# Optimization experiments

Measured on AMD Instinct MI355X. Metric: run time of the kernel, lower is better.

Reference implementation:

```python
import jax, jax.numpy as jnp
import numpy as np

B, T, H, UNITS = 64, 512, 1024, 1024

def setup_inputs() -> dict:
    key = jax.random.key(0)
    ks = jax.random.split(key, 8)
    s = 0.02
    return {
        "dec_hidden": jax.random.normal(ks[0], (B, H), jnp.float32),
        "enc_output": jax.random.normal(ks[1], (B, T, H), jnp.float32),
        "Wh": jax.random.normal(ks[2], (H, UNITS), jnp.float32) * s,
        "bh": jnp.zeros((UNITS,), jnp.float32),
        "Ws": jax.random.normal(ks[3], (H, UNITS), jnp.float32) * s,
        "bs": jnp.zeros((UNITS,), jnp.float32),
        "Wv": jax.random.normal(ks[4], (UNITS, 1), jnp.float32) * s,
        "bv": jnp.zeros((1,), jnp.float32),
    }

def reference(dec_hidden, enc_output, Wh, bh, Ws, bs, Wv, bv):
    # Faithful to original: tanh applied only to W_h(enc_output) term.
    enc_proj = jnp.tanh(jnp.einsum('bth,hu->btu', enc_output, Wh) + bh)  # [B,T,U]
    dec_proj = (dec_hidden @ Ws + bs)[:, None, :]                        # [B,1,U]
    score = jnp.einsum('btu,uo->bto', enc_proj + dec_proj, Wv) + bv      # [B,T,1]
    attn_dist = jax.nn.softmax(score, axis=1)                            # [B,T,1]
    context_vector = jnp.sum(attn_dist * enc_output, axis=1)             # [B,H]
    return context_vector, jnp.squeeze(attn_dist, axis=-1)
```

## Files before the change

### kernel.cpp

```cpp
#include <hip/hip_runtime.h>
#include <hip/hip_bf16.h>

typedef unsigned short u16;
typedef __attribute__((ext_vector_type(8))) short short8;
typedef __attribute__((ext_vector_type(4))) float f32x4;

#define B_  64
#define T_  512
#define H_  1024
#define U_  1024
#define BT_ (B_*T_)

#define BM 256
#define BN 256
#define BK 32

#define GLL16(gp, lp) __builtin_amdgcn_global_load_lds( \
    (const __attribute__((address_space(1))) void*)(gp), \
    (__attribute__((address_space(3))) void*)(lp), 16, 0, 0)

template<int N>
__device__ __forceinline__ void vwait() {
  asm volatile("s_waitcnt vmcnt(%0)" :: "n"(N) : "memory");
}

__device__ __forceinline__ u16 f32_to_bf16(float f) {
  union { float f; unsigned u; } v; v.f = f;
  unsigned r = v.u + 0x7FFFu + ((v.u >> 16) & 1u);
  return (u16)(r >> 16);
}
__device__ __forceinline__ unsigned pack_bf16x2(float lo, float hi) {
  return (unsigned)f32_to_bf16(lo) | ((unsigned)f32_to_bf16(hi) << 16);
}

__global__ __launch_bounds__(256) void ba_prep(const float4* __restrict__ in,
                                               uint4* __restrict__ out,
                                               const float* __restrict__ wh,
                                               u16* __restrict__ whT,
                                               float* __restrict__ score) {
  __shared__ float tile[32][33];
  const int bx = blockIdx.x;
  const int tid = threadIdx.x;
  if (bx < 16384) {
    int i = bx * 256 + tid;
    float4 v0 = in[2 * i], v1 = in[2 * i + 1];
    uint4 o;
    o.x = pack_bf16x2(v0.x, v0.y);
    o.y = pack_bf16x2(v0.z, v0.w);
    o.z = pack_bf16x2(v1.x, v1.y);
    o.w = pack_bf16x2(v1.z, v1.w);
    out[i] = o;
    if (bx < 128) score[bx * 256 + tid] = 0.f;
  } else {
    int wb = bx - 16384;
    int u0 = (wb & 31) * 32, h0 = (wb >> 5) * 32;
    int tx = tid & 31, ty = tid >> 5;
    #pragma unroll
    for (int i = 0; i < 32; i += 8)
      tile[ty + i][tx] = wh[(long)(h0 + ty + i) * U_ + u0 + tx];
    __syncthreads();
    #pragma unroll
    for (int i = 0; i < 32; i += 8)
      whT[(long)(u0 + ty + i) * H_ + h0 + tx] = f32_to_bf16(tile[tx][ty + i]);
  }
}

__global__ __launch_bounds__(512, 2) void ba_score(
    const u16* __restrict__ A, const u16* __restrict__ Bt,
    const float* __restrict__ bh, const float* __restrict__ wv,
    float* __restrict__ score) {
  __shared__ u16 lA[4][BM * BK];
  __shared__ u16 lB[4][BN * BK];

  const int tid  = threadIdx.x;
  const int wid  = tid >> 6;
  const int lane = tid & 63;
  const int wm = wid >> 2;
  const int wn = wid & 3;
  const long row0  = (long)blockIdx.x * BM;
  const int  ncol0 = blockIdx.y * BN;

  const int srow = tid >> 2;
  const int csw  = (((tid & 3) - ((tid >> 3) & 3)) & 3) * 8;

  const int fr = lane & 15;
  const int pofs = (((lane >> 4) + ((lane >> 1) & 3)) & 3) * 8;
  const int aBase = (wm * 128 + fr) * BK + pofs;
  const int bBase = (wn * 64  + fr) * BK + pofs;

  const u16* gA = A  + (row0 + srow) * H_ + csw;
  const u16* gB = Bt + (long)(ncol0 + srow) * H_ + csw;

  f32x4 acc[8][4];
  #pragma unroll
  for (int i = 0; i < 8; ++i)
    #pragma unroll
    for (int j = 0; j < 4; ++j) acc[i][j] = (f32x4){0.f, 0.f, 0.f, 0.f};

#define STAGEF(t_, b_) do { \
    const long _k = (long)(t_) * BK; \
    GLL16(gA + _k,            (char*)lA[b_] + wid * 1024); \
    GLL16(gA + 128 * H_ + _k, (char*)lA[b_] + 8192 + wid * 1024); \
    GLL16(gB + _k,            (char*)lB[b_] + wid * 1024); \
    GLL16(gB + 128 * H_ + _k, (char*)lB[b_] + 8192 + wid * 1024); \
  } while (0)

#define TILE(t_, WAITN, DO_STAGE) do { \
    const int _bt = (t_) & 3; \
    vwait<WAITN>(); \
    __builtin_amdgcn_sched_barrier(0); \
    __builtin_amdgcn_s_barrier(); \
    __builtin_amdgcn_sched_barrier(0); \
    short8 bfrag[4], afrag[4]; \
    _Pragma("unroll") \
    for (int nf = 0; nf < 4; ++nf) \
      bfrag[nf] = *(const short8*)&lB[_bt][bBase + nf * 512]; \
    _Pragma("unroll") \
    for (int mf = 0; mf < 4; ++mf) \
      afrag[mf] = *(const short8*)&lA[_bt][aBase + mf * 512]; \
    if (DO_STAGE) { \
      const long _k = (long)((t_) + 3) * BK; \
      const int _nb = ((t_) + 3) & 3; \
      GLL16(gA + _k,            (char*)lA[_nb] + wid * 1024); \
      GLL16(gA + 128 * H_ + _k, (char*)lA[_nb] + 8192 + wid * 1024); \
    } \
    __builtin_amdgcn_s_setprio(1); \
    _Pragma("unroll") \
    for (int mf = 0; mf < 4; ++mf) \
      _Pragma("unroll") \
      for (int nf = 0; nf < 4; ++nf) \
        acc[mf][nf] = __builtin_amdgcn_mfma_f32_16x16x32_bf16(afrag[mf], bfrag[nf], acc[mf][nf], 0, 0, 0); \
    __builtin_amdgcn_s_setprio(0); \
    _Pragma("unroll") \
    for (int mf = 0; mf < 4; ++mf) \
      afrag[mf] = *(const short8*)&lA[_bt][aBase + (4 + mf) * 512]; \
    if (DO_STAGE) { \
      const long _k = (long)((t_) + 3) * BK; \
      const int _nb = ((t_) + 3) & 3; \
      GLL16(gB + _k,            (char*)lB[_nb] + wid * 1024); \
      GLL16(gB + 128 * H_ + _k, (char*)lB[_nb] + 8192 + wid * 1024); \
    } \
    __builtin_amdgcn_s_setprio(1); \
    _Pragma("unroll") \
    for (int mf = 0; mf < 4; ++mf) \
      _Pragma("unroll") \
      for (int nf = 0; nf < 4; ++nf) \
        acc[4 + mf][nf] = __builtin_amdgcn_mfma_f32_16x16x32_bf16(afrag[mf], bfrag[nf], acc[4 + mf][nf], 0, 0, 0); \
    __builtin_amdgcn_s_setprio(0); \
  } while (0)

  STAGEF(0, 0);
  STAGEF(1, 1);
  STAGEF(2, 2);

  for (int t = 0; t < 30; ++t) {
    TILE(t, 8, t < 29);
  }
  TILE(30, 4, false);
  TILE(31, 0, false);
#undef TILE
#undef STAGEF

  float sloc[8][4];
  #pragma unroll
  for (int mf = 0; mf < 8; ++mf)
    #pragma unroll
    for (int r = 0; r < 4; ++r) sloc[mf][r] = 0.f;

  #pragma unroll
  for (int nf = 0; nf < 4; ++nf) {
    const int n = ncol0 + wn * 64 + nf * 16 + fr;
    const float bhn = bh[n];
    const float wvn = wv[n];
    #pragma unroll
    for (int mf = 0; mf < 8; ++mf) {
      #pragma unroll
      for (int r = 0; r < 4; ++r) {
        float x = acc[mf][nf][r] + bhn;
        float e = __expf(2.f * x);
        sloc[mf][r] += (1.f - 2.f / (e + 1.f)) * wvn;
      }
    }
  }

  #pragma unroll
  for (int mf = 0; mf < 8; ++mf) {
    #pragma unroll
    for (int r = 0; r < 4; ++r) {
      float v = sloc[mf][r];
      v += __shfl_xor(v, 1);
      v += __shfl_xor(v, 2);
      v += __shfl_xor(v, 4);
      v += __shfl_xor(v, 8);
      if ((lane & 15) == 0) {
        long m = row0 + wm * 128 + mf * 16 + (lane >> 4) * 4 + r;
        atomicAdd(&score[m], v);
      }
    }
  }
}

__global__ __launch_bounds__(256) void ba_context1(const float4* __restrict__ enc4,
                                                   const float* __restrict__ score,
                                                   float* __restrict__ attn_out,
                                                   float4* __restrict__ part) {
  __shared__ float redm[4], reds[4];
  __shared__ float atile[32];
  int b = blockIdx.x, c = blockIdx.y, tid = threadIdx.x;
  int lane = tid & 63, wid = tid >> 6;
  const float* s = score + b * T_;
  float v0 = s[tid], v1 = s[tid + 256];
  float m = fmaxf(v0, v1);
  #pragma unroll
  for (int o = 1; o < 64; o <<= 1) m = fmaxf(m, __shfl_xor(m, o));
  if (lane == 0) redm[wid] = m;
  __syncthreads();
  m = fmaxf(fmaxf(redm[0], redm[1]), fmaxf(redm[2], redm[3]));
  float e0 = __expf(v0 - m), e1 = __expf(v1 - m);
  float sum = e0 + e1;
  #pragma unroll
  for (int o = 1; o < 64; o <<= 1) sum += __shfl_xor(sum, o);
  if (lane == 0) reds[wid] = sum;
  __syncthreads();
  float inv = 1.f / (reds[0] + reds[1] + reds[2] + reds[3]);

  if (c == 0) {
    attn_out[b * T_ + tid] = e0 * inv;
    attn_out[b * T_ + tid + 256] = e1 * inv;
  }
  int base = c * 32;
  if (base < 256) {
    if (tid >= base && tid < base + 32) atile[tid - base] = e0 * inv;
  } else {
    int bb = base - 256;
    if (tid >= bb && tid < bb + 32) atile[tid - bb] = e1 * inv;
  }
  __syncthreads();

  const float4* e = enc4 + ((long)b * T_ + base) * (H_ / 4) + tid;
  float4 acc = {0.f, 0.f, 0.f, 0.f};
  #pragma unroll 4
  for (int t = 0; t < 32; ++t) {
    float4 v = e[(long)t * (H_ / 4)];
    float at = atile[t];
    acc.x = fmaf(at, v.x, acc.x);
    acc.y = fmaf(at, v.y, acc.y);
    acc.z = fmaf(at, v.z, acc.z);
    acc.w = fmaf(at, v.w, acc.w);
  }
  part[((long)b * 16 + c) * (H_ / 4) + tid] = acc;
}

__global__ __launch_bounds__(256) void ba_context2(const float4* __restrict__ part,
                                                   float4* __restrict__ ctx) {
  int b = blockIdx.x;
  int tid = threadIdx.x;
  const float4* p = part + (long)b * 16 * (H_ / 4) + tid;
  float4 acc = {0.f, 0.f, 0.f, 0.f};
  #pragma unroll
  for (int c = 0; c < 16; ++c) {
    float4 v = p[c * (H_ / 4)];
    acc.x += v.x; acc.y += v.y; acc.z += v.z; acc.w += v.w;
  }
  ctx[b * (H_ / 4) + tid] = acc;
}

extern "C" void kernel_launch(void* const* d_in, const int* in_sizes, int n_in,
                              void* d_out, int out_size, void* d_ws, size_t ws_size,
                              hipStream_t stream) {
  const float* enc = (const float*)d_in[1];
  const float* Wh  = (const float*)d_in[2];
  const float* bh  = (const float*)d_in[3];
  const float* Wv  = (const float*)d_in[6];

  float* out      = (float*)d_out;
  float* ctx_out  = out;
  float* attn_out = out + B_ * H_;

  char* ws = (char*)d_ws;
  u16*   encb  = (u16*)ws;
  u16*   whT   = (u16*)(ws + (size_t)67108864);
  float* score = (float*)(ws + (size_t)67108864 + 2097152);
  float* part  = (float*)(ws + (size_t)67108864 + 2097152 + 131072);

  ba_prep<<<16384 + 1024, 256, 0, stream>>>((const float4*)enc, (uint4*)encb,
                                            Wh, whT, score);
  ba_score<<<dim3(BT_ / BM, U_ / BN), 512, 0, stream>>>(encb, whT, bh, Wv, score);
  ba_context1<<<dim3(B_, 16), 256, 0, stream>>>((const float4*)enc, score,
                                                attn_out, (float4*)part);
  ba_context2<<<B_, 256, 0, stream>>>((const float4*)part, (float4*)ctx_out);
}
```

Before: 323.0 us.

## Switch score GEMM from 16x16x32 to 32x32x16 bf16 MFMA tiles

Replaces the 16x16x32 bf16 MFMA instruction with 32x32x16, reorganising each wave's 128x64 tile into 4x2 fragments of 32x32 with 16-wide accumulators. LDS fragment addressing, the k-half split within BK=32, and the epilogue row mapping and shuffle reduction (now across 32 lanes) are all reworked to match the new output layout. The larger MFMA shape halves the number of fragment loads per tile and may issue more efficiently, at the cost of a new LDS access pattern whose bank behaviour and swizzle correctness are less certain.

```diff
diff --git a/kernel.cpp b/kernel.cpp
--- a/kernel.cpp
+++ b/kernel.cpp
@@ -3,7 +3,7 @@
 
 typedef unsigned short u16;
 typedef __attribute__((ext_vector_type(8))) short short8;
-typedef __attribute__((ext_vector_type(4))) float f32x4;
+typedef __attribute__((ext_vector_type(16))) float f32x16;
 
 #define B_  64
 #define T_  512
@@ -83,19 +83,21 @@
   const int srow = tid >> 2;
   const int csw  = (((tid & 3) - ((tid >> 3) & 3)) & 3) * 8;
 
-  const int fr = lane & 15;
-  const int pofs = (((lane >> 4) + ((lane >> 1) & 3)) & 3) * 8;
-  const int aBase = (wm * 128 + fr) * BK + pofs;
-  const int bBase = (wn * 64  + fr) * BK + pofs;
+  const int l31 = lane & 31;
+  const int rowA = (wm * 128 + l31) * BK;
+  const int rowB = (wn * 64  + l31) * BK;
+  const int s0 = (((lane >> 5) + ((lane >> 1) & 3)) & 3) * 8;
 
   const u16* gA = A  + (row0 + srow) * H_ + csw;
   const u16* gB = Bt + (long)(ncol0 + srow) * H_ + csw;
 
-  f32x4 acc[8][4];
-  #pragma unroll
-  for (int i = 0; i < 8; ++i)
-    #pragma unroll
-    for (int j = 0; j < 4; ++j) acc[i][j] = (f32x4){0.f, 0.f, 0.f, 0.f};
+  f32x16 acc[4][2];
+  #pragma unroll
+  for (int i = 0; i < 4; ++i)
+    #pragma unroll
+    for (int j = 0; j < 2; ++j)
+      #pragma unroll
+      for (int r = 0; r < 16; ++r) acc[i][j][r] = 0.f;
 
 #define STAGEF(t_, b_) do { \
     const long _k = (long)(t_) * BK; \
@@ -111,13 +113,13 @@
     __builtin_amdgcn_sched_barrier(0); \
     __builtin_amdgcn_s_barrier(); \
     __builtin_amdgcn_sched_barrier(0); \
-    short8 bfrag[4], afrag[4]; \
-    _Pragma("unroll") \
-    for (int nf = 0; nf < 4; ++nf) \
-      bfrag[nf] = *(const short8*)&lB[_bt][bBase + nf * 512]; \
-    _Pragma("unroll") \
-    for (int mf = 0; mf < 4; ++mf) \
-      afrag[mf] = *(const short8*)&lA[_bt][aBase + mf * 512]; \
+    short8 af[4], bfr[2]; \
+    _Pragma("unroll") \
+    for (int mf = 0; mf < 4; ++mf) \
+      af[mf] = *(const short8*)&lA[_bt][rowA + mf * 1024 + s0]; \
+    _Pragma("unroll") \
+    for (int nf = 0; nf < 2; ++nf) \
+      bfr[nf] = *(const short8*)&lB[_bt][rowB + nf * 1024 + s0]; \
     if (DO_STAGE) { \
       const long _k = (long)((t_) + 3) * BK; \
       const int _nb = ((t_) + 3) & 3; \
@@ -128,12 +130,15 @@
     _Pragma("unroll") \
     for (int mf = 0; mf < 4; ++mf) \
       _Pragma("unroll") \
-      for (int nf = 0; nf < 4; ++nf) \
-        acc[mf][nf] = __builtin_amdgcn_mfma_f32_16x16x32_bf16(afrag[mf], bfrag[nf], acc[mf][nf], 0, 0, 0); \
+      for (int nf = 0; nf < 2; ++nf) \
+        acc[mf][nf] = __builtin_amdgcn_mfma_f32_32x32x16_bf16(af[mf], bfr[nf], acc[mf][nf], 0, 0, 0); \
     __builtin_amdgcn_s_setprio(0); \
     _Pragma("unroll") \
     for (int mf = 0; mf < 4; ++mf) \
-      afrag[mf] = *(const short8*)&lA[_bt][aBase + (4 + mf) * 512]; \
+      af[mf] = *(const short8*)&lA[_bt][rowA + mf * 1024 + (s0 ^ 16)]; \
+    _Pragma("unroll") \
+    for (int nf = 0; nf < 2; ++nf) \
+      bfr[nf] = *(const short8*)&lB[_bt][rowB + nf * 1024 + (s0 ^ 16)]; \
     if (DO_STAGE) { \
       const long _k = (long)((t_) + 3) * BK; \
       const int _nb = ((t_) + 3) & 3; \
@@ -144,8 +149,8 @@
     _Pragma("unroll") \
     for (int mf = 0; mf < 4; ++mf) \
       _Pragma("unroll") \
-      for (int nf = 0; nf < 4; ++nf) \
-        acc[4 + mf][nf] = __builtin_amdgcn_mfma_f32_16x16x32_bf16(afrag[mf], bfrag[nf], acc[4 + mf][nf], 0, 0, 0); \
+      for (int nf = 0; nf < 2; ++nf) \
+        acc[mf][nf] = __builtin_amdgcn_mfma_f32_32x32x16_bf16(af[mf], bfr[nf], acc[mf][nf], 0, 0, 0); \
     __builtin_amdgcn_s_setprio(0); \
   } while (0)
 
@@ -161,21 +166,21 @@
 #undef TILE
 #undef STAGEF
 
-  float sloc[8][4];
-  #pragma unroll
-  for (int mf = 0; mf < 8; ++mf)
-    #pragma unroll
-    for (int r = 0; r < 4; ++r) sloc[mf][r] = 0.f;
-
-  #pragma unroll
-  for (int nf = 0; nf < 4; ++nf) {
-    const int n = ncol0 + wn * 64 + nf * 16 + fr;
+  float sloc[4][16];
+  #pragma unroll
+  for (int mf = 0; mf < 4; ++mf)
+    #pragma unroll
+    for (int r = 0; r < 16; ++r) sloc[mf][r] = 0.f;
+
+  #pragma unroll
+  for (int nf = 0; nf < 2; ++nf) {
+    const int n = ncol0 + wn * 64 + nf * 32 + l31;
     const float bhn = bh[n];
     const float wvn = wv[n];
     #pragma unroll
-    for (int mf = 0; mf < 8; ++mf) {
+    for (int mf = 0; mf < 4; ++mf) {
       #pragma unroll
-      for (int r = 0; r < 4; ++r) {
+      for (int r = 0; r < 16; ++r) {
         float x = acc[mf][nf][r] + bhn;
         float e = __expf(2.f * x);
         sloc[mf][r] += (1.f - 2.f / (e + 1.f)) * wvn;
@@ -184,16 +189,17 @@
   }
 
   #pragma unroll
-  for (int mf = 0; mf < 8; ++mf) {
-    #pragma unroll
-    for (int r = 0; r < 4; ++r) {
+  for (int mf = 0; mf < 4; ++mf) {
+    #pragma unroll
+    for (int r = 0; r < 16; ++r) {
       float v = sloc[mf][r];
       v += __shfl_xor(v, 1);
       v += __shfl_xor(v, 2);
       v += __shfl_xor(v, 4);
       v += __shfl_xor(v, 8);
-      if ((lane & 15) == 0) {
-        long m = row0 + wm * 128 + mf * 16 + (lane >> 4) * 4 + r;
+      v += __shfl_xor(v, 16);
+      if (l31 == 0) {
+        long m = row0 + wm * 128 + mf * 32 + (r & 3) + 8 * (r >> 2) + 4 * (lane >> 5);
         atomicAdd(&score[m], v);
       }
     }
```

Measured after the change: 333.5 us. 1.03x slower.
